# Kernel optimization log

Measured on AMD Instinct MI355X. Metric: run time of the kernel, lower is better.

## Reference

```python
import jax, jax.numpy as jnp
import numpy as np

T, B = 128, 4096          # rollout length, num parallel envs
H = 128                   # lstm hidden
FEAT = 96                 # 32 (image) + 32 (loc) + 32 (energy)
NA = 6                    # num_actions
GRID, MAXE = 10.0, 200.0


def setup_inputs() -> dict:
    key = jax.random.key(0)
    ks = jax.random.split(key, 24)
    N = T * B
    w = lambda k, shp, s=0.05: (jax.random.normal(k, shp, jnp.float32) * s)
    return {
        "image": jax.random.uniform(ks[0], (N, 5, 5), jnp.float32),
        "location": jax.random.uniform(ks[1], (N, 2), jnp.float32),
        "energy": jax.random.uniform(ks[2], (N, 1), jnp.float32),
        "done": jax.random.randint(ks[3], (N,), 0, 2).astype(jnp.int32),
        "h0": jnp.zeros((B, H), jnp.float32),
        "c0": jnp.zeros((B, H), jnp.float32),
        # visual encoder MLP 25->256->256->128->32
        "W1": w(ks[4], (25, 256)),  "b1": jnp.zeros(256, jnp.float32),
        "W2": w(ks[5], (256, 256)), "b2": jnp.zeros(256, jnp.float32),
        "W3": w(ks[6], (256, 128)), "b3": jnp.zeros(128, jnp.float32),
        "W4": w(ks[7], (128, 32)),  "b4": jnp.zeros(32, jnp.float32),
        # location / energy encoders
        "Wl": w(ks[8], (2, 32)), "bl": jnp.zeros(32, jnp.float32),
        "We": w(ks[9], (1, 32)), "be": jnp.zeros(32, jnp.float32),
        # LSTM (PyTorch layout: gates [i,f,g,o], W_ih: [4H, in], W_hh: [4H, H])
        "Wih": w(ks[10], (4 * H, FEAT)), "Whh": w(ks[11], (4 * H, H)),
        "bih": jnp.zeros(4 * H, jnp.float32), "bhh": jnp.zeros(4 * H, jnp.float32),
        # actor / critic heads
        "Wa": w(ks[12], (H, NA)), "ba": jnp.zeros(NA, jnp.float32),
        "Wc": w(ks[13], (H, 1)),  "bc": jnp.zeros(1, jnp.float32),
    }


def _forward(image, location, energy, done, h0, c0,
             W1, b1, W2, b2, W3, b3, W4, b4, Wl, bl, We, be,
             Wih, Whh, bih, bhh, Wa, ba, Wc, bc):
    relu = jax.nn.relu
    x = image.reshape(-1, 25) / 255.0                      # [N,25]
    f = relu(x @ W1 + b1)
    f = relu(f @ W2 + b2)
    f = relu(f @ W3 + b3)
    img_feat = relu(f @ W4 + b4)                           # [N,32]
    loc_feat = (location / GRID) @ Wl + bl                 # [N,32]
    eng_feat = (energy / MAXE) @ We + be                   # [N,32]
    feats = jnp.concatenate([img_feat, loc_feat, eng_feat], axis=1)  # [N,96]
    xs = feats.reshape(T, B, FEAT)
    ds = done.astype(jnp.float32).reshape(T, B)
    bias = bih + bhh                                       # [4H]

    def step(carry, inp):
        h, c = carry                                       # [B,H]
        x_t, d_t = inp
        mask = (1.0 - d_t)[:, None]                        # reset on done
        h = h * mask
        c = c * mask
        gates = x_t @ Wih.T + h @ Whh.T + bias             # [B,4H]
        i, fg, g, o = jnp.split(gates, 4, axis=1)
        c = jax.nn.sigmoid(fg) * c + jax.nn.sigmoid(i) * jnp.tanh(g)
        h = jax.nn.sigmoid(o) * jnp.tanh(c)
        return (h, c), h

    (hT, cT), hs = jax.lax.scan(step, (h0, c0), (xs, ds))  # hs: [T,B,H]
    hidden = hs.reshape(-1, H)                             # [N,H]
    logits = hidden @ Wa + ba                              # [N,NA]
    value = hidden @ Wc + bc                               # [N,1]
    return jnp.concatenate([logits, value], axis=1)        # [N,NA+1]


def reference(image, location, energy, done, h0, c0,
              W1, b1, W2, b2, W3, b3, W4, b4, Wl, bl, We, be,
              Wih, Whh, bih, bhh, Wa, ba, Wc, bc):
    return _forward(image, location, energy, done, h0, c0,
                    W1, b1, W2, b2, W3, b3, W4, b4, Wl, bl, We, be,
                    Wih, Whh, bih, bhh, Wa, ba, Wc, bc)
```

## Files before the change

kernel.cpp:

```cpp
#include <hip/hip_runtime.h>

#define T_ 128
#define B_ 4096
#define N_ (T_*B_)
#define H_ 128
#define FEAT_ 96
#define K_ 224
#define G4H_ 512
#define L2E 1.4426950408889634f

typedef __attribute__((ext_vector_type(8))) short short8;
typedef __attribute__((ext_vector_type(4))) short short4v;
typedef __attribute__((ext_vector_type(4))) float f32x4;

__device__ __forceinline__ float sig2(float x) {
    return __builtin_amdgcn_rcpf(1.0f + __builtin_amdgcn_exp2f(-x));
}
__device__ __forceinline__ float ftanh(float x) {
    float e = __builtin_amdgcn_exp2f(-2.0f * L2E * x);
    return fmaf(2.0f, __builtin_amdgcn_rcpf(1.0f + e), -1.0f);
}
__device__ __forceinline__ short f2bf(float f) {
    unsigned u = __builtin_bit_cast(unsigned, f);
    u += 0x7fff + ((u >> 16) & 1);
    return (short)(u >> 16);
}
__device__ __forceinline__ short4v pack4relu(const f32x4 a) {
    short4v v;
    v[0] = f2bf(fmaxf(a[0], 0.f)); v[1] = f2bf(fmaxf(a[1], 0.f));
    v[2] = f2bf(fmaxf(a[2], 0.f)); v[3] = f2bf(fmaxf(a[3], 0.f));
    return v;
}

#define FBASE(t, grp, kk) ((((size_t)(t) * 256 + (grp)) * 3 + (kk)) * 512)

__global__ __launch_bounds__(256) void prep_kernel(
    const float* __restrict__ Wih, const float* __restrict__ Whh,
    const float* __restrict__ bih, const float* __restrict__ bhh,
    const float* __restrict__ W1, const float* __restrict__ W2,
    const float* __restrict__ W3, const float* __restrict__ W4,
    short* __restrict__ Wtp, float* __restrict__ bias,
    short* __restrict__ W1p, short* __restrict__ W2p,
    short* __restrict__ W3p, short* __restrict__ W4p)
{
    int idx = blockIdx.x * 256 + threadIdx.x;
    if (idx < 114688) {
        int j = idx & 7, L = (idx >> 3) & 63, r = idx >> 9;
        int kk = r % 7, n = r / 7;
        int k = kk * 32 + ((L >> 4) << 3) + j;
        int g = (n << 4) + (L & 15);
        float v = (k < FEAT_) ? Wih[g * FEAT_ + k] : Whh[g * H_ + (k - FEAT_)];
        float s = (n >= 16 && n < 24) ? (2.0f * L2E) : L2E;
        Wtp[idx] = f2bf(v * s);
        return;
    }
    int e = idx - 114688;
    if (e < 8192) {
        int j = e & 7, L = (e >> 3) & 63, nt = e >> 9;
        int k = ((L >> 4) << 3) + j;
        int o = nt * 16 + (L & 15);
        W1p[e] = (k < 25) ? f2bf(W1[k * 256 + o] * (1.0f / 255.0f)) : (short)0;
        return;
    }
    e -= 8192;
    if (e < 65536) {
        int j = e & 7, L = (e >> 3) & 63, f = e >> 9;
        int kk = f & 7, nt = f >> 3;
        int k = kk * 32 + ((L >> 4) << 3) + j;
        W2p[e] = f2bf(W2[k * 256 + nt * 16 + (L & 15)]);
        return;
    }
    e -= 65536;
    if (e < 32768) {
        int j = e & 7, L = (e >> 3) & 63, f = e >> 9;
        int kk = f & 7, nt = f >> 3;
        int k = kk * 32 + ((L >> 4) << 3) + j;
        W3p[e] = f2bf(W3[k * 128 + nt * 16 + (L & 15)]);
        return;
    }
    e -= 32768;
    if (e < 4096) {
        int j = e & 7, L = (e >> 3) & 63, f = e >> 9;
        int kk = f & 3, nt = f >> 2;
        int k = kk * 32 + ((L >> 4) << 3) + j;
        W4p[e] = f2bf(W4[k * 32 + nt * 16 + (L & 15)]);
        return;
    }
    e -= 4096;
    if (e < 512) {
        float s = ((e >> 7) == 2) ? (2.0f * L2E) : L2E;
        bias[e] = (bih[e] + bhh[e]) * s;
    }
}

__global__ __launch_bounds__(256) void loc_kernel(
    const float* __restrict__ location, const float* __restrict__ energy,
    const float* __restrict__ Wl, const float* __restrict__ bl,
    const float* __restrict__ We, const float* __restrict__ be,
    short* __restrict__ featsb)
{
    __shared__ float C[160];
    const int tid = threadIdx.x;
    if (tid < 160) {
        float v;
        if (tid < 64)       v = Wl[tid];
        else if (tid < 96)  v = bl[tid - 64];
        else if (tid < 128) v = We[tid - 96];
        else                v = be[tid - 128];
        C[tid] = v;
    }
    __syncthreads();
    const int n = blockIdx.x * 64 + (tid >> 2);
    const int p = tid & 3;
    const float lx = location[(size_t)n * 2 + 0] * 0.1f;
    const float ly = location[(size_t)n * 2 + 1] * 0.1f;
    const float ev = energy[n] * (1.0f / 200.0f);
    const int t = n >> 12, b = n & 4095;
    const int grp = b >> 4, bi = b & 15;
    const int kk = 1 + (p >> 1);
    #pragma unroll
    for (int o = 0; o < 2; o++) {
        const int f0 = 32 + p * 16 + o * 8;
        short8 v;
        #pragma unroll
        for (int j = 0; j < 8; j++) {
            const int f = f0 + j;
            float val;
            if (f < 64) { const int cix = f - 32; val = fmaf(lx, C[cix], fmaf(ly, C[32 + cix], C[64 + cix])); }
            else        { const int cix = f - 64; val = fmaf(ev, C[96 + cix], C[128 + cix]); }
            v[j] = f2bf(val);
        }
        const int Lhi = ((p & 1) << 1) + o;
        *(short8*)&featsb[FBASE(t, grp, kk) + (Lhi * 16 + bi) * 8] = v;
    }
}

__global__ __launch_bounds__(512, 2) void enc_kernel(
    const float* __restrict__ image,
    const short* __restrict__ W1p, const float* __restrict__ b1,
    const short* __restrict__ W2p, const float* __restrict__ b2,
    const short* __restrict__ W3p, const float* __restrict__ b3,
    const short* __restrict__ W4p, const float* __restrict__ b4,
    short* __restrict__ featsb)
{
    __shared__ float Raw[2][800];
    __shared__ __align__(16) short In[2 * 512];
    __shared__ __align__(16) short AA[2 * 8 * 512];
    __shared__ __align__(16) short AB[2 * 8 * 512];
    __shared__ __align__(16) short AC[2 * 4 * 512];
    const int tid  = threadIdx.x;
    const int lane = tid & 63, wv = tid >> 6;
    const int col  = lane & 15, quad = lane >> 4;

    short8 w1r[2], w2r[2][8], w3r[8], w4r[4];
    #pragma unroll
    for (int i = 0; i < 2; i++)
        w1r[i] = *(const short8*)&W1p[((wv + 8 * i) * 64 + lane) * 8];
    #pragma unroll
    for (int i = 0; i < 2; i++)
        #pragma unroll
        for (int kk = 0; kk < 8; kk++)
            w2r[i][kk] = *(const short8*)&W2p[(((wv + 8 * i) * 8 + kk) * 64 + lane) * 8];
    #pragma unroll
    for (int kk = 0; kk < 8; kk++)
        w3r[kk] = *(const short8*)&W3p[((wv * 8 + kk) * 64 + lane) * 8];
    #pragma unroll
    for (int kk = 0; kk < 4; kk++)
        w4r[kk] = *(const short8*)&W4p[(((wv & 1) * 4 + kk) * 64 + lane) * 8];
    float4 b1r[2], b2r[2];
    #pragma unroll
    for (int i = 0; i < 2; i++) {
        b1r[i] = *(const float4*)(b1 + (wv + 8 * i) * 16 + quad * 4);
        b2r[i] = *(const float4*)(b2 + (wv + 8 * i) * 16 + quad * 4);
    }
    const float4 b3r = *(const float4*)(b3 + wv * 16 + quad * 4);
    const float4 b4r = *(const float4*)(b4 + (wv & 1) * 16 + quad * 4);

    const bool ld = tid < 400;
    const int w4t = tid - 256;
    float2 ir = {0.f, 0.f};

    if (ld) {
        float2 t0 = *(const float2*)(image + (size_t)blockIdx.x * 800 + 2 * tid);
        Raw[0][2 * tid] = t0.x; Raw[0][2 * tid + 1] = t0.y;
        ir = *(const float2*)(image + (size_t)(blockIdx.x + 256) * 800 + 2 * tid);
    }
    __syncthreads();
    if (w4t >= 0 && w4t < 128) {
        const int st = w4t >> 6, L = w4t & 63;
        const int s = st * 16 + (L & 15), kb = (L >> 4) * 8;
        short8 v;
        #pragma unroll
        for (int j = 0; j < 8; j++) {
            const int kx = kb + j;
            v[j] = (kx < 25) ? f2bf(Raw[0][s * 25 + kx]) : (short)0;
        }
        *(short8*)&In[(st * 64 + L) * 8] = v;
    }

    for (int it = 0; it < 64; it++) {
        const int nxt = (it & 1) ^ 1;
        const int tile = it * 256 + blockIdx.x;
        if (ld && it + 1 < 64) { Raw[nxt][2 * tid] = ir.x; Raw[nxt][2 * tid + 1] = ir.y; }
        if (ld && it + 2 < 64)
            ir = *(const float2*)(image + (size_t)(tile + 512) * 800 + 2 * tid);
        __syncthreads();

        {
            short8 bx[2];
            #pragma unroll
            for (int st = 0; st < 2; st++) bx[st] = *(const short8*)&In[(st * 64 + lane) * 8];
            #pragma unroll
            for (int i = 0; i < 2; i++) {
                const int nt = wv + 8 * i;
                #pragma unroll
                for (int st = 0; st < 2; st++) {
                    f32x4 acc = (f32x4){b1r[i].x, b1r[i].y, b1r[i].z, b1r[i].w};
                    acc = __builtin_amdgcn_mfma_f32_16x16x32_bf16(w1r[i], bx[st], acc, 0, 0, 0);
                    *(short4v*)&AA[((st * 8 + (nt >> 1)) * 64 + ((((nt & 1) << 1) + (quad >> 1)) << 4) + col) * 8 + (quad & 1) * 4]
                        = pack4relu(acc);
                }
            }
        }
        __syncthreads();

        {
            f32x4 acc[2][2];
            #pragma unroll
            for (int i = 0; i < 2; i++)
                #pragma unroll
                for (int st = 0; st < 2; st++)
                    acc[i][st] = (f32x4){b2r[i].x, b2r[i].y, b2r[i].z, b2r[i].w};
            #pragma unroll
            for (int kk = 0; kk < 8; kk++) {
                short8 bx[2];
                #pragma unroll
                for (int st = 0; st < 2; st++)
                    bx[st] = *(const short8*)&AA[((st * 8 + kk) * 64 + lane) * 8];
                #pragma unroll
                for (int i = 0; i < 2; i++)
                    #pragma unroll
                    for (int st = 0; st < 2; st++)
                        acc[i][st] = __builtin_amdgcn_mfma_f32_16x16x32_bf16(w2r[i][kk], bx[st], acc[i][st], 0, 0, 0);
            }
            #pragma unroll
            for (int i = 0; i < 2; i++) {
                const int nt = wv + 8 * i;
                #pragma unroll
                for (int st = 0; st < 2; st++)
                    *(short4v*)&AB[((st * 8 + (nt >> 1)) * 64 + ((((nt & 1) << 1) + (quad >> 1)) << 4) + col) * 8 + (quad & 1) * 4]
                        = pack4relu(acc[i][st]);
            }
        }
        __syncthreads();

        {
            f32x4 acc[2];
            #pragma unroll
            for (int st = 0; st < 2; st++) acc[st] = (f32x4){b3r.x, b3r.y, b3r.z, b3r.w};
            #pragma unroll
            for (int kk = 0; kk < 8; kk++) {
                #pragma unroll
                for (int st = 0; st < 2; st++) {
                    const short8 bx = *(const short8*)&AB[((st * 8 + kk) * 64 + lane) * 8];
                    acc[st] = __builtin_amdgcn_mfma_f32_16x16x32_bf16(w3r[kk], bx, acc[st], 0, 0, 0);
                }
            }
            const int nt = wv;
            #pragma unroll
            for (int st = 0; st < 2; st++)
                *(short4v*)&AC[((st * 4 + (nt >> 1)) * 64 + ((((nt & 1) << 1) + (quad >> 1)) << 4) + col) * 8 + (quad & 1) * 4]
                    = pack4relu(acc[st]);
        }
        __syncthreads();

        if (wv < 4) {
            const int nt = wv & 1, st = wv >> 1;
            f32x4 acc = (f32x4){b4r.x, b4r.y, b4r.z, b4r.w};
            #pragma unroll
            for (int kk = 0; kk < 4; kk++) {
                const short8 bx = *(const short8*)&AC[((st * 4 + kk) * 64 + lane) * 8];
                acc = __builtin_amdgcn_mfma_f32_16x16x32_bf16(w4r[kk], bx, acc, 0, 0, 0);
            }
            const int t4 = tile >> 7;
            const int grp = (tile & 127) * 2 + st;
            *(short4v*)&featsb[FBASE(t4, grp, 0) + (((nt << 1) + (quad >> 1)) * 16 + col) * 8 + (quad & 1) * 4]
                = pack4relu(acc);
        } else if (w4t >= 0 && w4t < 128 && it + 1 < 64) {
            const int st = w4t >> 6, L = w4t & 63;
            const int s = st * 16 + (L & 15), kb = (L >> 4) * 8;
            short8 v;
            #pragma unroll
            for (int j = 0; j < 8; j++) {
                const int kx = kb + j;
                v[j] = (kx < 25) ? f2bf(Raw[nxt][s * 25 + kx]) : (short)0;
            }
            *(short8*)&In[(st * 64 + L) * 8] = v;
        }
    }
}

__global__ __launch_bounds__(512, 2) void lstm_kernel(
    const short* __restrict__ featsb, const int* __restrict__ done,
    const float* __restrict__ h0, const float* __restrict__ c0,
    const short* __restrict__ Wtp, const float* __restrict__ bias,
    const float* __restrict__ Wa, const float* __restrict__ ba,
    const float* __restrict__ Wc, const float* __restrict__ bc,
    float* __restrict__ out)
{
    __shared__ __align__(16) short Hb[2][4 * 64 * 8];
    __shared__ __align__(16) short HW[4 * 64 * 8];
    __shared__ float Ml[T_ * 16];

    const int tid = threadIdx.x;
    const int r0 = blockIdx.x * 16;
    const int grp = r0 >> 4;
    const int lane = tid & 63;
    const int wv = tid >> 6;
    const int col = lane & 15;
    const int quad = lane >> 4;
    const int u = (wv << 4) + col;

    short8 wtr[4][7];
    #pragma unroll
    for (int g = 0; g < 4; g++)
        #pragma unroll
        for (int kk = 0; kk < 7; kk++)
            wtr[g][kk] = *(const short8*)&Wtp[((size_t)((wv + 8 * g) * 7 + kk) * 64 + lane) * 8];

    for (int idx = tid; idx < 4 * 64 * 8; idx += 512) {
        int j = idx & 7, L = (idx >> 3) & 63, kk2 = idx >> 9;
        int k = kk2 * 32 + ((L >> 4) << 3) + j;
        int n = L & 15;
        float v = (n < 6) ? Wa[k * 6 + n] : (n == 6 ? Wc[k] : 0.0f);
        HW[idx] = f2bf(v);
    }
    for (int idx = tid; idx < T_ * 16; idx += 512)
        Ml[idx] = 1.0f - (float)done[(size_t)(idx >> 4) * B_ + r0 + (idx & 15)];

    const int kk2h = wv >> 1;
    const int Lhi_h = ((wv & 1) << 1) | (col >> 3);
    const int jh = col & 7;
    f32x4 c;
    #pragma unroll
    for (int r = 0; r < 4; r++) {
        const int s = (quad << 2) + r;
        const float m = 1.0f - (float)done[r0 + s];
        c[r] = c0[(size_t)(r0 + s) * H_ + u] * m;
        Hb[0][(kk2h * 64 + Lhi_h * 16 + s) * 8 + jh] = f2bf(h0[(size_t)(r0 + s) * H_ + u]);
    }
    const float bi0 = bias[((wv +  0) << 4) + col];
    const float bi1 = bias[((wv +  8) << 4) + col];
    const float bi2 = bias[((wv + 16) << 4) + col];
    const float bi3 = bias[((wv + 24) << 4) + col];
    const float hb = (col < 6) ? ba[col] : (col == 6 ? bc[0] : 0.0f);

    short8 xa[3], xb[3];
    #pragma unroll
    for (int kk = 0; kk < 3; kk++) {
        xa[kk] = *(const short8*)&featsb[FBASE(0, grp, kk) + lane * 8];
        xb[kk] = *(const short8*)&featsb[FBASE(1, grp, kk) + lane * 8];
    }
    __syncthreads();

    auto STEP = [&](int t, int cur, short8* X) {
        const int nxt = cur ^ 1;
        const float mcol = Ml[t * 16 + col];
        f32x4 acc0 = {bi0, bi0, bi0, bi0};
        f32x4 acc1 = {bi1, bi1, bi1, bi1};
        f32x4 acc2 = {bi2, bi2, bi2, bi2};
        f32x4 acc3 = {bi3, bi3, bi3, bi3};
        #pragma unroll
        for (int kk = 0; kk < 7; kk++) {
            short8 af;
            if (kk < 3) af = X[kk];
            else {
                af = *(const short8*)&Hb[cur][((kk - 3) * 64 + lane) * 8];
                if (mcol == 0.0f) af = (short8){0,0,0,0,0,0,0,0};
            }
            acc0 = __builtin_amdgcn_mfma_f32_16x16x32_bf16(af, wtr[0][kk], acc0, 0, 0, 0);
            acc1 = __builtin_amdgcn_mfma_f32_16x16x32_bf16(af, wtr[1][kk], acc1, 0, 0, 0);
            acc2 = __builtin_amdgcn_mfma_f32_16x16x32_bf16(af, wtr[2][kk], acc2, 0, 0, 0);
            acc3 = __builtin_amdgcn_mfma_f32_16x16x32_bf16(af, wtr[3][kk], acc3, 0, 0, 0);
        }
        float4 mn = {1.f, 1.f, 1.f, 1.f};
        if (t < T_ - 1) mn = *(const float4*)&Ml[(t + 1) * 16 + (quad << 2)];
        #pragma unroll
        for (int r = 0; r < 4; r++) {
            const float ig = sig2(acc0[r]);
            const float fg = sig2(acc1[r]);
            const float gt = fmaf(2.0f, sig2(acc2[r]), -1.0f);
            const float og = sig2(acc3[r]);
            const float cn = fmaf(fg, c[r], ig * gt);
            const float h = og * ftanh(cn);
            c[r] = cn * ((&mn.x)[r]);
            Hb[nxt][(kk2h * 64 + Lhi_h * 16 + (quad << 2) + r) * 8 + jh] = f2bf(h);
        }
        if (t + 2 < T_) {
            #pragma unroll
            for (int kk = 0; kk < 3; kk++)
                X[kk] = *(const short8*)&featsb[FBASE(t + 2, grp, kk) + lane * 8];
        }
        __syncthreads();

        if (wv == (t & 7)) {
            f32x4 ha = {hb, hb, hb, hb};
            #pragma unroll
            for (int kk2 = 0; kk2 < 4; kk2++) {
                const short8 hf = *(const short8*)&Hb[nxt][(kk2 * 64 + lane) * 8];
                const short8 wf = *(const short8*)&HW[(kk2 * 64 + lane) * 8];
                ha = __builtin_amdgcn_mfma_f32_16x16x32_bf16(hf, wf, ha, 0, 0, 0);
            }
            if (col < 7) {
                #pragma unroll
                for (int r = 0; r < 4; r++) {
                    const int s = (quad << 2) + r;
                    out[((size_t)t * B_ + r0 + s) * 7 + col] = ha[r];
                }
            }
        }
    };

    for (int t = 0; t < T_; t += 2) {
        STEP(t, 0, xa);
        STEP(t + 1, 1, xb);
    }
}

extern "C" void kernel_launch(void* const* d_in, const int* in_sizes, int n_in,
                              void* d_out, int out_size, void* d_ws, size_t ws_size,
                              hipStream_t stream) {
    const float* image    = (const float*)d_in[0];
    const float* location = (const float*)d_in[1];
    const float* energy   = (const float*)d_in[2];
    const int*   done     = (const int*)d_in[3];
    const float* h0       = (const float*)d_in[4];
    const float* c0       = (const float*)d_in[5];
    const float* W1 = (const float*)d_in[6];   const float* b1 = (const float*)d_in[7];
    const float* W2 = (const float*)d_in[8];   const float* b2 = (const float*)d_in[9];
    const float* W3 = (const float*)d_in[10];  const float* b3 = (const float*)d_in[11];
    const float* W4 = (const float*)d_in[12];  const float* b4 = (const float*)d_in[13];
    const float* Wl = (const float*)d_in[14];  const float* bl = (const float*)d_in[15];
    const float* We = (const float*)d_in[16];  const float* be = (const float*)d_in[17];
    const float* Wih = (const float*)d_in[18]; const float* Whh = (const float*)d_in[19];
    const float* bih = (const float*)d_in[20]; const float* bhh = (const float*)d_in[21];
    const float* Wa = (const float*)d_in[22];  const float* ba = (const float*)d_in[23];
    const float* Wc = (const float*)d_in[24];  const float* bc = (const float*)d_in[25];

    char* ws = (char*)d_ws;
    short* Wtp   = (short*)ws;
    float* bias  = (float*)(ws + 229376);
    short* W1p   = (short*)(ws + 231424);
    short* W2p   = (short*)(ws + 247808);
    short* W3p   = (short*)(ws + 378880);
    short* W4p   = (short*)(ws + 444416);
    short* featsb = (short*)(ws + 452608);
    float* out   = (float*)d_out;

    prep_kernel<<<882, 256, 0, stream>>>(Wih, Whh, bih, bhh, W1, W2, W3, W4,
                                         Wtp, bias, W1p, W2p, W3p, W4p);
    loc_kernel<<<N_ / 64, 256, 0, stream>>>(location, energy, Wl, bl, We, be, featsb);
    enc_kernel<<<256, 512, 0, stream>>>(image, W1p, b1, W2p, b2, W3p, b3, W4p, b4, featsb);
    lstm_kernel<<<B_ / 16, 512, 0, stream>>>(featsb, done, h0, c0, Wtp, bias,
                                             Wa, ba, Wc, bc, out);
}
```

Baseline: 427.6 us.

## Fuse location/energy encoder into enc kernel and batch LSTM head outputs over steps

Removes the separate loc_kernel launch by computing the location/energy features inside enc_kernel before its main loop. In the LSTM kernel the hidden-state buffer grows from two to sixteen slots, so the actor/critic head runs once every eight steps with all eight waves busy, instead of one wave per step. The input-feature MFMAs are also issued before the featsb prefetch and the recurrent part, so global loads overlap compute. The cost is more LDS for the hidden history, which may lower occupancy, and an extra barrier in the encoder loop.

```diff
diff --git a/kernel.cpp b/kernel.cpp
--- a/kernel.cpp
+++ b/kernel.cpp
@@ -93,50 +93,11 @@
     }
 }
 
-__global__ __launch_bounds__(256) void loc_kernel(
+__global__ __launch_bounds__(512, 2) void enc_kernel(
+    const float* __restrict__ image,
     const float* __restrict__ location, const float* __restrict__ energy,
     const float* __restrict__ Wl, const float* __restrict__ bl,
     const float* __restrict__ We, const float* __restrict__ be,
-    short* __restrict__ featsb)
-{
-    __shared__ float C[160];
-    const int tid = threadIdx.x;
-    if (tid < 160) {
-        float v;
-        if (tid < 64)       v = Wl[tid];
-        else if (tid < 96)  v = bl[tid - 64];
-        else if (tid < 128) v = We[tid - 96];
-        else                v = be[tid - 128];
-        C[tid] = v;
-    }
-    __syncthreads();
-    const int n = blockIdx.x * 64 + (tid >> 2);
-    const int p = tid & 3;
-    const float lx = location[(size_t)n * 2 + 0] * 0.1f;
-    const float ly = location[(size_t)n * 2 + 1] * 0.1f;
-    const float ev = energy[n] * (1.0f / 200.0f);
-    const int t = n >> 12, b = n & 4095;
-    const int grp = b >> 4, bi = b & 15;
-    const int kk = 1 + (p >> 1);
-    #pragma unroll
-    for (int o = 0; o < 2; o++) {
-        const int f0 = 32 + p * 16 + o * 8;
-        short8 v;
-        #pragma unroll
-        for (int j = 0; j < 8; j++) {
-            const int f = f0 + j;
-            float val;
-            if (f < 64) { const int cix = f - 32; val = fmaf(lx, C[cix], fmaf(ly, C[32 + cix], C[64 + cix])); }
-            else        { const int cix = f - 64; val = fmaf(ev, C[96 + cix], C[128 + cix]); }
-            v[j] = f2bf(val);
-        }
-        const int Lhi = ((p & 1) << 1) + o;
-        *(short8*)&featsb[FBASE(t, grp, kk) + (Lhi * 16 + bi) * 8] = v;
-    }
-}
-
-__global__ __launch_bounds__(512, 2) void enc_kernel(
-    const float* __restrict__ image,
     const short* __restrict__ W1p, const float* __restrict__ b1,
     const short* __restrict__ W2p, const float* __restrict__ b2,
     const short* __restrict__ W3p, const float* __restrict__ b3,
@@ -148,6 +109,7 @@
     __shared__ __align__(16) short AA[2 * 8 * 512];
     __shared__ __align__(16) short AB[2 * 8 * 512];
     __shared__ __align__(16) short AC[2 * 4 * 512];
+    __shared__ float C[160];
     const int tid  = threadIdx.x;
     const int lane = tid & 63, wv = tid >> 6;
     const int col  = lane & 15, quad = lane >> 4;
@@ -176,35 +138,75 @@
     const float4 b3r = *(const float4*)(b3 + wv * 16 + quad * 4);
     const float4 b4r = *(const float4*)(b4 + (wv & 1) * 16 + quad * 4);
 
+    if (tid < 160) {
+        float v;
+        if (tid < 64)       v = Wl[tid];
+        else if (tid < 96)  v = bl[tid - 64];
+        else if (tid < 128) v = We[tid - 96];
+        else                v = be[tid - 128];
+        C[tid] = v;
+    }
+
     const bool ld = tid < 400;
-    const int w4t = tid - 256;
     float2 ir = {0.f, 0.f};
-
     if (ld) {
         float2 t0 = *(const float2*)(image + (size_t)blockIdx.x * 800 + 2 * tid);
         Raw[0][2 * tid] = t0.x; Raw[0][2 * tid + 1] = t0.y;
         ir = *(const float2*)(image + (size_t)(blockIdx.x + 256) * 800 + 2 * tid);
     }
     __syncthreads();
-    if (w4t >= 0 && w4t < 128) {
-        const int st = w4t >> 6, L = w4t & 63;
-        const int s = st * 16 + (L & 15), kb = (L >> 4) * 8;
-        short8 v;
-        #pragma unroll
-        for (int j = 0; j < 8; j++) {
-            const int kx = kb + j;
-            v[j] = (kx < 25) ? f2bf(Raw[0][s * 25 + kx]) : (short)0;
-        }
-        *(short8*)&In[(st * 64 + L) * 8] = v;
+
+    for (int q = tid; q < 2048; q += 512) {
+        const int itq = q >> 5, s = q & 31;
+        const int n = (itq * 256 + blockIdx.x) * 32 + s;
+        const float lx = location[(size_t)n * 2 + 0] * 0.1f;
+        const float ly = location[(size_t)n * 2 + 1] * 0.1f;
+        const float ev = energy[n] * (1.0f / 200.0f);
+        const int t = n >> 12, b = n & 4095;
+        const int grp = b >> 4, bi = b & 15;
+        #pragma unroll
+        for (int p = 0; p < 4; p++) {
+            const int kk = 1 + (p >> 1);
+            #pragma unroll
+            for (int o = 0; o < 2; o++) {
+                const int f0 = 32 + p * 16 + o * 8;
+                short8 v;
+                #pragma unroll
+                for (int j = 0; j < 8; j++) {
+                    const int f = f0 + j;
+                    float val;
+                    if (f < 64) { const int cix = f - 32; val = fmaf(lx, C[cix], fmaf(ly, C[32 + cix], C[64 + cix])); }
+                    else        { const int cix = f - 64; val = fmaf(ev, C[96 + cix], C[128 + cix]); }
+                    v[j] = f2bf(val);
+                }
+                const int Lhi = ((p & 1) << 1) + o;
+                *(short8*)&featsb[FBASE(t, grp, kk) + (Lhi * 16 + bi) * 8] = v;
+            }
+        }
+    }
+
+    {
+        const int w4t = tid - 256;
+        if (w4t >= 0 && w4t < 128) {
+            const int st = w4t >> 6, L = w4t & 63;
+            const int s = st * 16 + (L & 15), kb = (L >> 4) * 8;
+            short8 v;
+            #pragma unroll
+            for (int j = 0; j < 8; j++) {
+                const int kx = kb + j;
+                v[j] = (kx < 25) ? f2bf(Raw[0][s * 25 + kx]) : (short)0;
+            }
+            *(short8*)&In[(st * 64 + L) * 8] = v;
+        }
     }
 
     for (int it = 0; it < 64; it++) {
         const int nxt = (it & 1) ^ 1;
         const int tile = it * 256 + blockIdx.x;
         if (ld && it + 1 < 64) { Raw[nxt][2 * tid] = ir.x; Raw[nxt][2 * tid + 1] = ir.y; }
+        __syncthreads();
         if (ld && it + 2 < 64)
             ir = *(const float2*)(image + (size_t)(tile + 512) * 800 + 2 * tid);
-        __syncthreads();
 
         {
             short8 bx[2];
@@ -286,16 +288,19 @@
             const int grp = (tile & 127) * 2 + st;
             *(short4v*)&featsb[FBASE(t4, grp, 0) + (((nt << 1) + (quad >> 1)) * 16 + col) * 8 + (quad & 1) * 4]
                 = pack4relu(acc);
-        } else if (w4t >= 0 && w4t < 128 && it + 1 < 64) {
-            const int st = w4t >> 6, L = w4t & 63;
-            const int s = st * 16 + (L & 15), kb = (L >> 4) * 8;
-            short8 v;
-            #pragma unroll
-            for (int j = 0; j < 8; j++) {
-                const int kx = kb + j;
-                v[j] = (kx < 25) ? f2bf(Raw[nxt][s * 25 + kx]) : (short)0;
-            }
-            *(short8*)&In[(st * 64 + L) * 8] = v;
+        } else {
+            const int w4t = tid - 256;
+            if (w4t >= 0 && w4t < 128 && it + 1 < 64) {
+                const int st = w4t >> 6, L = w4t & 63;
+                const int s = st * 16 + (L & 15), kb = (L >> 4) * 8;
+                short8 v;
+                #pragma unroll
+                for (int j = 0; j < 8; j++) {
+                    const int kx = kb + j;
+                    v[j] = (kx < 25) ? f2bf(Raw[nxt][s * 25 + kx]) : (short)0;
+                }
+                *(short8*)&In[(st * 64 + L) * 8] = v;
+            }
         }
     }
 }
@@ -308,7 +313,7 @@
     const float* __restrict__ Wc, const float* __restrict__ bc,
     float* __restrict__ out)
 {
-    __shared__ __align__(16) short Hb[2][4 * 64 * 8];
+    __shared__ __align__(16) short Hb[16][4 * 64 * 8];
     __shared__ __align__(16) short HW[4 * 64 * 8];
     __shared__ float Ml[T_ * 16];
 
@@ -347,7 +352,7 @@
         const int s = (quad << 2) + r;
         const float m = 1.0f - (float)done[r0 + s];
         c[r] = c0[(size_t)(r0 + s) * H_ + u] * m;
-        Hb[0][(kk2h * 64 + Lhi_h * 16 + s) * 8 + jh] = f2bf(h0[(size_t)(r0 + s) * H_ + u]);
+        Hb[15][(kk2h * 64 + Lhi_h * 16 + s) * 8 + jh] = f2bf(h0[(size_t)(r0 + s) * H_ + u]);
     }
     const float bi0 = bias[((wv +  0) << 4) + col];
     const float bi1 = bias[((wv +  8) << 4) + col];
@@ -363,21 +368,31 @@
     }
     __syncthreads();
 
-    auto STEP = [&](int t, int cur, short8* X) {
-        const int nxt = cur ^ 1;
+    auto STEP = [&](int t, short8* X) {
+        const int rs = (t + 15) & 15;
+        const int ws = t & 15;
         const float mcol = Ml[t * 16 + col];
         f32x4 acc0 = {bi0, bi0, bi0, bi0};
         f32x4 acc1 = {bi1, bi1, bi1, bi1};
         f32x4 acc2 = {bi2, bi2, bi2, bi2};
         f32x4 acc3 = {bi3, bi3, bi3, bi3};
         #pragma unroll
-        for (int kk = 0; kk < 7; kk++) {
-            short8 af;
-            if (kk < 3) af = X[kk];
-            else {
-                af = *(const short8*)&Hb[cur][((kk - 3) * 64 + lane) * 8];
-                if (mcol == 0.0f) af = (short8){0,0,0,0,0,0,0,0};
-            }
+        for (int kk = 0; kk < 3; kk++) {
+            const short8 af = X[kk];
+            acc0 = __builtin_amdgcn_mfma_f32_16x16x32_bf16(af, wtr[0][kk], acc0, 0, 0, 0);
+            acc1 = __builtin_amdgcn_mfma_f32_16x16x32_bf16(af, wtr[1][kk], acc1, 0, 0, 0);
+            acc2 = __builtin_amdgcn_mfma_f32_16x16x32_bf16(af, wtr[2][kk], acc2, 0, 0, 0);
+            acc3 = __builtin_amdgcn_mfma_f32_16x16x32_bf16(af, wtr[3][kk], acc3, 0, 0, 0);
+        }
+        if (t + 2 < T_) {
+            #pragma unroll
+            for (int kk = 0; kk < 3; kk++)
+                X[kk] = *(const short8*)&featsb[FBASE(t + 2, grp, kk) + lane * 8];
+        }
+        #pragma unroll
+        for (int kk = 3; kk < 7; kk++) {
+            short8 af = *(const short8*)&Hb[rs][((kk - 3) * 64 + lane) * 8];
+            if (mcol == 0.0f) af = (short8){0,0,0,0,0,0,0,0};
             acc0 = __builtin_amdgcn_mfma_f32_16x16x32_bf16(af, wtr[0][kk], acc0, 0, 0, 0);
             acc1 = __builtin_amdgcn_mfma_f32_16x16x32_bf16(af, wtr[1][kk], acc1, 0, 0, 0);
             acc2 = __builtin_amdgcn_mfma_f32_16x16x32_bf16(af, wtr[2][kk], acc2, 0, 0, 0);
@@ -394,20 +409,17 @@
             const float cn = fmaf(fg, c[r], ig * gt);
             const float h = og * ftanh(cn);
             c[r] = cn * ((&mn.x)[r]);
-            Hb[nxt][(kk2h * 64 + Lhi_h * 16 + (quad << 2) + r) * 8 + jh] = f2bf(h);
-        }
-        if (t + 2 < T_) {
-            #pragma unroll
-            for (int kk = 0; kk < 3; kk++)
-                X[kk] = *(const short8*)&featsb[FBASE(t + 2, grp, kk) + lane * 8];
+            Hb[ws][(kk2h * 64 + Lhi_h * 16 + (quad << 2) + r) * 8 + jh] = f2bf(h);
         }
         __syncthreads();
 
-        if (wv == (t & 7)) {
+        if ((t & 7) == 7) {
+            const int tp = t - 7 + wv;
+            const int sp = tp & 15;
             f32x4 ha = {hb, hb, hb, hb};
             #pragma unroll
             for (int kk2 = 0; kk2 < 4; kk2++) {
-                const short8 hf = *(const short8*)&Hb[nxt][(kk2 * 64 + lane) * 8];
+                const short8 hf = *(const short8*)&Hb[sp][(kk2 * 64 + lane) * 8];
                 const short8 wf = *(const short8*)&HW[(kk2 * 64 + lane) * 8];
                 ha = __builtin_amdgcn_mfma_f32_16x16x32_bf16(hf, wf, ha, 0, 0, 0);
             }
@@ -415,15 +427,15 @@
                 #pragma unroll
                 for (int r = 0; r < 4; r++) {
                     const int s = (quad << 2) + r;
-                    out[((size_t)t * B_ + r0 + s) * 7 + col] = ha[r];
+                    out[((size_t)tp * B_ + r0 + s) * 7 + col] = ha[r];
                 }
             }
         }
     };
 
     for (int t = 0; t < T_; t += 2) {
-        STEP(t, 0, xa);
-        STEP(t + 1, 1, xb);
+        STEP(t, xa);
+        STEP(t + 1, xb);
     }
 }
 
@@ -459,8 +471,8 @@
 
     prep_kernel<<<882, 256, 0, stream>>>(Wih, Whh, bih, bhh, W1, W2, W3, W4,
                                          Wtp, bias, W1p, W2p, W3p, W4p);
-    loc_kernel<<<N_ / 64, 256, 0, stream>>>(location, energy, Wl, bl, We, be, featsb);
-    enc_kernel<<<256, 512, 0, stream>>>(image, W1p, b1, W2p, b2, W3p, b3, W4p, b4, featsb);
+    enc_kernel<<<256, 512, 0, stream>>>(image, location, energy, Wl, bl, We, be,
+                                        W1p, b1, W2p, b2, W3p, b3, W4p, b4, featsb);
     lstm_kernel<<<B_ / 16, 512, 0, stream>>>(featsb, done, h0, c0, Wtp, bias,
                                              Wa, ba, Wc, bc, out);
 }
```

Measured after the change: 662.8 us. +55.0%, slower.
